# Kernel tuning notes

Measured on AMD Instinct MI355X. Metric: run time of the kernel, lower is better.

## Reference

```python
import jax, jax.numpy as jnp
import numpy as np

N = 100_000   # nodes
E = 1_250_000 # edges
D = 64        # node feature dim
H = 64        # hidden_channels
C = 10        # num_classes
G = 128       # graphs in batch


def setup_inputs() -> dict:
    key = jax.random.key(0)
    ks = jax.random.split(key, 12)
    x = jax.random.normal(ks[0], (N, D), dtype=jnp.float32)
    edge_index = jax.random.randint(ks[1], (2, E), 0, N, dtype=jnp.int64)
    batch = jnp.sort(jax.random.randint(ks[2], (N,), 0, G, dtype=jnp.int64))
    s = lambda fan_in: 1.0 / np.sqrt(fan_in)
    W1 = jax.random.normal(ks[3], (D, H), dtype=jnp.float32) * s(D)
    b1 = jnp.zeros((H,), dtype=jnp.float32)
    W2 = jax.random.normal(ks[4], (H, H), dtype=jnp.float32) * s(H)
    b2 = jnp.zeros((H,), dtype=jnp.float32)
    W3 = jax.random.normal(ks[5], (H, H), dtype=jnp.float32) * s(H)
    b3 = jnp.zeros((H,), dtype=jnp.float32)
    Wl = jax.random.normal(ks[6], (H, C), dtype=jnp.float32) * s(H)
    bl = jnp.zeros((C,), dtype=jnp.float32)
    return {"x": x, "edge_index": edge_index, "batch": batch,
            "W1": W1, "b1": b1, "W2": W2, "b2": b2,
            "W3": W3, "b3": b3, "Wl": Wl, "bl": bl}


def _gcn_conv(h, W, b, src, dst, norm, n_nodes):
    # GCNConv: out[i] = sum_{e: dst(e)=i} norm_e * (h @ W)[src(e)] + b
    h = h @ W
    msg = h[src] * norm[:, None]                       # [E+N, H]
    return jax.ops.segment_sum(msg, dst, num_segments=n_nodes) + b


def reference(x, edge_index, batch, W1, b1, W2, b2, W3, b3, Wl, bl):
    x = x.astype(jnp.float32)
    ei = edge_index.astype(jnp.int64)
    # add self-loops (as PyG gcn_norm does by default)
    loop = jnp.arange(N, dtype=ei.dtype)
    src = jnp.concatenate([ei[0], loop])
    dst = jnp.concatenate([ei[1], loop])
    # symmetric normalization: deg over targets (in-degree incl. self-loops)
    deg = jax.ops.segment_sum(jnp.ones_like(src, dtype=jnp.float32), dst,
                              num_segments=N)
    dinv = jnp.where(deg > 0, jax.lax.rsqrt(jnp.maximum(deg, 1.0)), 0.0)
    norm = dinv[src] * dinv[dst]                       # [E+N]

    h = jax.nn.relu(_gcn_conv(x, W1, b1, src, dst, norm, N))
    h = jax.nn.relu(_gcn_conv(h, W2, b2, src, dst, norm, N))
    h = _gcn_conv(h, W3, b3, src, dst, norm, N)

    # global_mean_pool over graph ids
    ones = jnp.ones((N,), dtype=jnp.float32)
    counts = jax.ops.segment_sum(ones, batch, num_segments=G)
    sums = jax.ops.segment_sum(h, batch, num_segments=G)
    pooled = sums / jnp.maximum(counts, 1.0)[:, None]  # [G, H]

    # dropout is identity in eval mode
    return pooled @ Wl + bl                            # [G, C]
```

## Files before the change

### kernel.cpp

```cpp
#include <hip/hip_runtime.h>
#include <hip/hip_bf16.h>


#define BSHIFT 7
#define BNODES (1 << BSHIFT)
#define EPB    8192
#define MAXDEG 8192
#define MAXBUCKET 32768

typedef __attribute__((ext_vector_type(8))) short bf16x8;
typedef __attribute__((ext_vector_type(4))) float f32x4;

__device__ __forceinline__ void atomAddF(float* p, float v) {
#if defined(__gfx90a__) || defined(__gfx940__) || defined(__gfx941__) || defined(__gfx942__) || defined(__gfx950__)
    unsafeAtomicAdd(p, v);
#else
    atomicAdd(p, v);
#endif
}

__device__ __forceinline__ unsigned short f2bf(float x) {
    unsigned u = __float_as_uint(x);
    u += 0x7FFFu + ((u >> 16) & 1u);
    return (unsigned short)(u >> 16);
}
__device__ __forceinline__ float bf2f(unsigned short b) {
    return __uint_as_float((unsigned)b << 16);
}

__global__ __launch_bounds__(256)
void k_bhist(const int* __restrict__ dst, int* __restrict__ cnt_all,
             int nE, int nBuckets, int binBlocks,
             const float* __restrict__ W1, const float* __restrict__ W2,
             const float* __restrict__ W3, unsigned short* __restrict__ Wt,
             float* __restrict__ pool, int poolN) {
    if (blockIdx.x >= binBlocks) {
        int li = blockIdx.x - binBlocks;
        if (li < 3) {
            const float* W = (li == 0) ? W1 : ((li == 1) ? W2 : W3);
            unsigned short* o = Wt + li * 4096;
            for (int idx = threadIdx.x; idx < 4096; idx += 256) {
                int h = idx >> 6, k = idx & 63;
                o[idx] = f2bf(W[k * 64 + h]);
            }
        } else {
            for (int i = threadIdx.x; i < poolN; i += 256) pool[i] = 0.f;
        }
        return;
    }
    __shared__ int cnt[1024];
    const int t = threadIdx.x;
    const int blk = blockIdx.x * EPB;
    for (int b = t; b < nBuckets; b += 256) cnt[b] = 0;
    __syncthreads();
#pragma unroll 4
    for (int i = 0; i < EPB / 256; i++) {
        int e = blk + i * 256 + t;
        if (e < nE) atomicAdd(&cnt[dst[e] >> BSHIFT], 1);
    }
    __syncthreads();
    for (int b = t; b < nBuckets; b += 256)
        cnt_all[(size_t)blockIdx.x * nBuckets + b] = cnt[b];
}

__global__ __launch_bounds__(256)
void k_colscan(int* __restrict__ cnt_all, int* __restrict__ bcnt,
               int nBlocks, int nBuckets) {
    const int lane = threadIdx.x & 63;
    const int b = blockIdx.x * 4 + (threadIdx.x >> 6);
    if (b >= nBuckets) return;
    int running = 0;
    for (int c = 0; c < nBlocks; c += 64) {
        int blk = c + lane;
        int v = (blk < nBlocks) ? cnt_all[(size_t)blk * nBuckets + b] : 0;
        int incl = v;
#pragma unroll
        for (int off = 1; off < 64; off <<= 1) {
            int tv = __shfl_up(incl, off);
            if (lane >= off) incl += tv;
        }
        if (blk < nBlocks) cnt_all[(size_t)blk * nBuckets + b] = running + (incl - v);
        running += __shfl(incl, 63);
    }
    if (lane == 0) bcnt[b] = running;
}

__global__ void k_bscan(const int* __restrict__ bcnt, int* __restrict__ bbase,
                        int nb, int nE) {
    __shared__ int s[256];
    const int t = threadIdx.x;
    const int base = t * 4;
    int v0 = (base + 0 < nb) ? bcnt[base + 0] : 0;
    int v1 = (base + 1 < nb) ? bcnt[base + 1] : 0;
    int v2 = (base + 2 < nb) ? bcnt[base + 2] : 0;
    int v3 = (base + 3 < nb) ? bcnt[base + 3] : 0;
    int tsum = v0 + v1 + v2 + v3;
    s[t] = tsum;
    __syncthreads();
    for (int off = 1; off < 256; off <<= 1) {
        int val = 0;
        if (t >= off) val = s[t - off];
        __syncthreads();
        if (t >= off) s[t] += val;
        __syncthreads();
    }
    int excl = s[t] - tsum;
    if (base + 0 < nb) bbase[base + 0] = excl;
    if (base + 1 < nb) bbase[base + 1] = excl + v0;
    if (base + 2 < nb) bbase[base + 2] = excl + v0 + v1;
    if (base + 3 < nb) bbase[base + 3] = excl + v0 + v1 + v2;
    if (t == 0) bbase[nb] = nE;
}

__global__ __launch_bounds__(256)
void k_bucket(const int* __restrict__ src, const int* __restrict__ dst,
              const int* __restrict__ bbase, const int* __restrict__ cnt_all,
              int* __restrict__ staging, int nE, int nBuckets) {
    __shared__ int cnt[1024];
    __shared__ int lbase[1024];
    const int t = threadIdx.x;
    const int blk = blockIdx.x * EPB;

    for (int b = t; b < nBuckets; b += 256) {
        lbase[b] = bbase[b] + cnt_all[(size_t)blockIdx.x * nBuckets + b];
        cnt[b] = 0;
    }
    __syncthreads();
#pragma unroll 4
    for (int i = 0; i < EPB / 256; i++) {
        int e = blk + i * 256 + t;
        if (e < nE) {
            int s0 = src[e], d0 = dst[e];
            int b = d0 >> BSHIFT;
            int off = atomicAdd(&cnt[b], 1);
            int pos = lbase[b] + off;
            if ((unsigned)pos < (unsigned)nE)
                staging[pos] = (s0 << BSHIFT) | (d0 & (BNODES - 1));
        }
    }
}

__global__ __launch_bounds__(256)
void k_sort(const int* __restrict__ staging, const int* __restrict__ bbase,
            int* __restrict__ csr_s, int* __restrict__ rowptr,
            int* __restrict__ rowend, float* __restrict__ dinv,
            int n, int nE) {
    __shared__ int c[BNODES];
    __shared__ int sc[BNODES];
    __shared__ int cur[BNODES];
    const int t = threadIdx.x;
    const int b = blockIdx.x;
    const int node0 = b << BSHIFT;

    int seg0 = bbase[b];
    int seg1 = bbase[b + 1];
    seg0 = max(0, min(seg0, nE));
    seg1 = max(seg0, min(seg1, nE));
    seg1 = min(seg1, seg0 + MAXBUCKET);

    if (t < BNODES) c[t] = 0;
    __syncthreads();
    for (int e = seg0 + t; e < seg1; e += 256)
        atomicAdd(&c[staging[e] & (BNODES - 1)], 1);
    __syncthreads();
    if (t < BNODES) sc[t] = c[t];
    __syncthreads();
    for (int off = 1; off < BNODES; off <<= 1) {
        int v = 0;
        if (t >= off && t < BNODES) v = sc[t - off];
        __syncthreads();
        if (t >= off && t < BNODES) sc[t] += v;
        __syncthreads();
    }
    if (t < BNODES) {
        int excl = sc[t] - c[t];
        cur[t] = excl;
        int node = node0 + t;
        if (node < n) {
            rowptr[node] = seg0 + excl;
            rowend[node] = seg0 + excl + c[t];
            dinv[node]   = rsqrtf((float)c[t] + 1.0f);
        }
    }
    __syncthreads();
    for (int e = seg0 + t; e < seg1; e += 256) {
        int p = staging[e];
        int l = p & (BNODES - 1);
        int pos = seg0 + atomicAdd(&cur[l], 1);
        if ((unsigned)pos < (unsigned)nE)
            csr_s[pos] = ((unsigned)p) >> BSHIFT;
    }
}

template<bool RELU, typename AT>
__device__ __forceinline__
void gemm_body(int bid, const AT* __restrict__ in,
               const unsigned short* __restrict__ Wt,
               const float* __restrict__ bias,
               unsigned short* __restrict__ out, int n) {
    const int lane = threadIdx.x & 63;
    const int wid  = threadIdx.x >> 6;
    const int col  = lane & 15;
    const int quad = lane >> 4;
    const int node0w = bid * 64 + wid * 16;
    const int nodeA  = node0w + col;
    const bool validA = nodeA < n;

    f32x4 zero4 = {0.f, 0.f, 0.f, 0.f};
    f32x4 acc0 = zero4, acc1 = zero4, acc2 = zero4, acc3 = zero4;

#pragma unroll
    for (int ks = 0; ks < 64; ks += 32) {
        const int kb = ks + quad * 8;
        float a[8];
        if constexpr (sizeof(AT) == 4) {
            float4 a0 = make_float4(0.f, 0.f, 0.f, 0.f);
            float4 a1 = make_float4(0.f, 0.f, 0.f, 0.f);
            if (validA) {
                a0 = *(const float4*)((const float*)in + (size_t)nodeA * 64 + kb);
                a1 = *(const float4*)((const float*)in + (size_t)nodeA * 64 + kb + 4);
            }
            a[0] = a0.x; a[1] = a0.y; a[2] = a0.z; a[3] = a0.w;
            a[4] = a1.x; a[5] = a1.y; a[6] = a1.z; a[7] = a1.w;
        } else {
            ushort4 h0 = make_ushort4(0, 0, 0, 0), h1 = make_ushort4(0, 0, 0, 0);
            if (validA) {
                h0 = *(const ushort4*)((const unsigned short*)in + (size_t)nodeA * 64 + kb);
                h1 = *(const ushort4*)((const unsigned short*)in + (size_t)nodeA * 64 + kb + 4);
            }
            a[0] = bf2f(h0.x); a[1] = bf2f(h0.y); a[2] = bf2f(h0.z); a[3] = bf2f(h0.w);
            a[4] = bf2f(h1.x); a[5] = bf2f(h1.y); a[6] = bf2f(h1.z); a[7] = bf2f(h1.w);
        }
        if (RELU) {
#pragma unroll
            for (int i = 0; i < 8; i++) a[i] = fmaxf(a[i] + bias[kb + i], 0.f);
        }
        bf16x8 af;
#pragma unroll
        for (int i = 0; i < 8; i++) af[i] = (short)f2bf(a[i]);

        const bf16x8 b0f = *(const bf16x8*)(Wt + ((0 * 16 + col) * 64 + kb));
        const bf16x8 b1f = *(const bf16x8*)(Wt + ((1 * 16 + col) * 64 + kb));
        const bf16x8 b2f = *(const bf16x8*)(Wt + ((2 * 16 + col) * 64 + kb));
        const bf16x8 b3f = *(const bf16x8*)(Wt + ((3 * 16 + col) * 64 + kb));
        acc0 = __builtin_amdgcn_mfma_f32_16x16x32_bf16(af, b0f, acc0, 0, 0, 0);
        acc1 = __builtin_amdgcn_mfma_f32_16x16x32_bf16(af, b1f, acc1, 0, 0, 0);
        acc2 = __builtin_amdgcn_mfma_f32_16x16x32_bf16(af, b2f, acc2, 0, 0, 0);
        acc3 = __builtin_amdgcn_mfma_f32_16x16x32_bf16(af, b3f, acc3, 0, 0, 0);
    }

#pragma unroll
    for (int r = 0; r < 4; r++) {
        int nn = node0w + quad * 4 + r;
        if (nn < n) {
            size_t base = (size_t)nn * 64 + col;
            out[base +  0] = f2bf(acc0[r]);
            out[base + 16] = f2bf(acc1[r]);
            out[base + 32] = f2bf(acc2[r]);
            out[base + 48] = f2bf(acc3[r]);
        }
    }
}

template<bool RELU, typename AT>
__global__ __launch_bounds__(256)
void k_gemm(const AT* __restrict__ in, const unsigned short* __restrict__ Wt,
            const float* __restrict__ bias, unsigned short* __restrict__ out, int n) {
    gemm_body<RELU, AT>(blockIdx.x, in, Wt, bias, out, n);
}

__global__ __launch_bounds__(256)
void k_wfgemm1(const int* __restrict__ csr_s, const float* __restrict__ dinv,
               float* __restrict__ csr_w, int nE, int n, int wfB,
               const float* __restrict__ x, const unsigned short* __restrict__ Wt,
               unsigned short* __restrict__ hW) {
    if (blockIdx.x < wfB) {
        int e = blockIdx.x * 256 + threadIdx.x;
        if (e < nE) {
            int s = csr_s[e];
            s = max(0, min(s, n - 1));
            csr_w[e] = dinv[s];
        }
        return;
    }
    gemm_body<false, float>(blockIdx.x - wfB, x, Wt, nullptr, hW, n);
}

template<int LAYER>
__global__ __launch_bounds__(256)
void k_agg(const unsigned short* __restrict__ hW, const int* __restrict__ rowptr,
           const int* __restrict__ rowend, const int* __restrict__ csr_s,
           const float* __restrict__ csr_w, const float* __restrict__ dinv,
           unsigned short* __restrict__ aggb, int n, int nE) {
    const int lane = threadIdx.x & 63;
    const int wid  = threadIdx.x >> 6;
    const int nA = blockIdx.x * 8 + wid * 2;
    const int nB = nA + 1;
    if (nA >= n) return;
    const bool vB = (nB < n);

    int rowA = rowptr[nA], endA = rowend[nA];
    rowA = max(0, min(rowA, nE)); endA = max(rowA, min(endA, nE));
    endA = min(endA, rowA + MAXDEG);
    int rowB = 0, endB = 0;
    if (vB) {
        rowB = rowptr[nB]; endB = rowend[nB];
        rowB = max(0, min(rowB, nE)); endB = max(rowB, min(endB, nE));
        endB = min(endB, rowB + MAXDEG);
    }
    const float diA = dinv[nA];
    const float diB = vB ? dinv[nB] : 0.f;

    float a0 = diA * diA * bf2f(hW[(size_t)nA * 64 + lane]);
    float a1 = 0.f, a2 = 0.f, a3 = 0.f;
    float b0 = vB ? diB * diB * bf2f(hW[(size_t)nB * 64 + lane]) : 0.f;
    float b1 = 0.f, b2 = 0.f, b3 = 0.f;

    const int nm1 = n - 1;
    int baseA = rowA, baseB = rowB;
    while (baseA < endA || baseB < endB) {
        int mA = max(0, min(32, endA - baseA));
        int mB = max(0, min(32, endB - baseB));
        int   s_l = 0;
        float w_l = 0.f;
        if (lane < 32) {
            if (lane < mA) {
                int e = baseA + lane;
                s_l = csr_s[e];
                w_l = csr_w[e] * diA;
            }
        } else {
            int l2 = lane - 32;
            if (l2 < mB) {
                int e = baseB + l2;
                s_l = csr_s[e];
                w_l = csr_w[e] * diB;
            }
        }
        const unsigned w_u = __float_as_uint(w_l);
        const int m = max(mA, mB);
        int j = 0;
        for (; j + 4 <= m; j += 4) {
            int sA0 = min(__builtin_amdgcn_readlane(s_l, j    ), nm1);
            int sA1 = min(__builtin_amdgcn_readlane(s_l, j + 1), nm1);
            int sA2 = min(__builtin_amdgcn_readlane(s_l, j + 2), nm1);
            int sA3 = min(__builtin_amdgcn_readlane(s_l, j + 3), nm1);
            int sB0 = min(__builtin_amdgcn_readlane(s_l, j + 32), nm1);
            int sB1 = min(__builtin_amdgcn_readlane(s_l, j + 33), nm1);
            int sB2 = min(__builtin_amdgcn_readlane(s_l, j + 34), nm1);
            int sB3 = min(__builtin_amdgcn_readlane(s_l, j + 35), nm1);
            float wA0 = __uint_as_float(__builtin_amdgcn_readlane(w_u, j));
            float wA1 = __uint_as_float(__builtin_amdgcn_readlane(w_u, j + 1));
            float wA2 = __uint_as_float(__builtin_amdgcn_readlane(w_u, j + 2));
            float wA3 = __uint_as_float(__builtin_amdgcn_readlane(w_u, j + 3));
            float wB0 = __uint_as_float(__builtin_amdgcn_readlane(w_u, j + 32));
            float wB1 = __uint_as_float(__builtin_amdgcn_readlane(w_u, j + 33));
            float wB2 = __uint_as_float(__builtin_amdgcn_readlane(w_u, j + 34));
            float wB3 = __uint_as_float(__builtin_amdgcn_readlane(w_u, j + 35));
            float hA0 = bf2f(hW[(size_t)sA0 * 64 + lane]);
            float hA1 = bf2f(hW[(size_t)sA1 * 64 + lane]);
            float hA2 = bf2f(hW[(size_t)sA2 * 64 + lane]);
            float hA3 = bf2f(hW[(size_t)sA3 * 64 + lane]);
            float hB0 = bf2f(hW[(size_t)sB0 * 64 + lane]);
            float hB1 = bf2f(hW[(size_t)sB1 * 64 + lane]);
            float hB2 = bf2f(hW[(size_t)sB2 * 64 + lane]);
            float hB3 = bf2f(hW[(size_t)sB3 * 64 + lane]);
            a0 += wA0 * hA0; a1 += wA1 * hA1;
            a2 += wA2 * hA2; a3 += wA3 * hA3;
            b0 += wB0 * hB0; b1 += wB1 * hB1;
            b2 += wB2 * hB2; b3 += wB3 * hB3;
        }
        for (; j < m; j++) {
            int   sA = min(__builtin_amdgcn_readlane(s_l, j), nm1);
            int   sB = min(__builtin_amdgcn_readlane(s_l, j + 32), nm1);
            float wA = __uint_as_float(__builtin_amdgcn_readlane(w_u, j));
            float wB = __uint_as_float(__builtin_amdgcn_readlane(w_u, j + 32));
            a0 += wA * bf2f(hW[(size_t)sA * 64 + lane]);
            b0 += wB * bf2f(hW[(size_t)sB * 64 + lane]);
        }
        baseA += mA;
        baseB += mB;
    }
    aggb[(size_t)nA * 64 + lane] = f2bf((a0 + a1) + (a2 + a3));
    if (vB) aggb[(size_t)nB * 64 + lane] = f2bf((b0 + b1) + (b2 + b3));
}

__global__ void k_pool(const unsigned short* __restrict__ aggb,
                       const int* __restrict__ batch,
                       float* __restrict__ pool, float* __restrict__ cnt, int n) {
    const int lane = threadIdx.x;
    const int base = blockIdx.x * 64;
    int g_cur = -1, run = 0;
    float acc = 0.f;
    for (int j = 0; j < 64; j++) {
        int node = base + j;
        if (node >= n) break;
        int g = batch[node];
        if (g != g_cur) {
            if (g_cur >= 0) {
                atomAddF(&pool[g_cur * 64 + lane], acc);
                if (lane == 0) atomAddF(&cnt[g_cur], (float)run);
            }
            g_cur = g; acc = 0.f; run = 0;
        }
        acc += bf2f(aggb[(size_t)node * 64 + lane]);
        run++;
    }
    if (g_cur >= 0) {
        atomAddF(&pool[g_cur * 64 + lane], acc);
        if (lane == 0) atomAddF(&cnt[g_cur], (float)run);
    }
}

__global__ void k_final(const float* __restrict__ pool, const float* __restrict__ cnt,
                        const float* __restrict__ b3, const float* __restrict__ Wl,
                        const float* __restrict__ bl, float* __restrict__ out) {
    __shared__ float s[64];
    const int g = blockIdx.x, t = threadIdx.x;
    float c = fmaxf(cnt[g], 1.0f);
    s[t] = pool[g * 64 + t] / c + b3[t];
    __syncthreads();
    if (t < 10) {
        float acc = bl[t];
#pragma unroll
        for (int k = 0; k < 64; k++) acc += s[k] * Wl[k * 10 + t];
        out[g * 10 + t] = acc;
    }
}

extern "C" void kernel_launch(void* const* d_in, const int* in_sizes, int n_in,
                              void* d_out, int out_size, void* d_ws, size_t ws_size,
                              hipStream_t stream) {
    const float* x   = (const float*)d_in[0];
    const int*   ei  = (const int*)d_in[1];
    const int*   bat = (const int*)d_in[2];
    const float* W1  = (const float*)d_in[3];
    const float* b1  = (const float*)d_in[4];
    const float* W2  = (const float*)d_in[5];
    const float* b2  = (const float*)d_in[6];
    const float* W3  = (const float*)d_in[7];
    const float* b3  = (const float*)d_in[8];
    const float* Wl  = (const float*)d_in[9];
    const float* bl  = (const float*)d_in[10];
    float* out = (float*)d_out;

    const int N_ = in_sizes[0] / 64;
    const int E_ = in_sizes[1] / 2;
    const int G_ = out_size / 10;
    const int NB_ = (N_ + BNODES - 1) >> BSHIFT;
    const int bin_blocks = (E_ + EPB - 1) / EPB;

    char* p = (char*)d_ws;
    int*   staging = (int*)p;   p += (size_t)E_ * 4;
    int*   csr_s  = (int*)p;    p += (size_t)E_ * 4;
    float* csr_w  = (float*)p;  p += (size_t)E_ * 4;
    unsigned short* aggb = (unsigned short*)p; p += (size_t)N_ * 64 * 2;
    unsigned short* hW   = (unsigned short*)p; p += (size_t)N_ * 64 * 2;
    float* dinv   = (float*)p;  p += (size_t)N_ * 4;
    int*   rowptr = (int*)p;    p += (size_t)N_ * 4;
    int*   rowend = (int*)p;    p += (size_t)N_ * 4;
    float* pool   = (float*)p;  p += (size_t)G_ * 64 * 4;
    float* cnt    = (float*)p;  p += (size_t)G_ * 4;
    unsigned short* Wt = (unsigned short*)p; p += 3 * 4096 * 2;
    int*   bcnt   = (int*)p;    p += (size_t)(NB_ + 1) * 4;
    int*   bbase  = (int*)p;    p += (size_t)(NB_ + 1) * 4;
    int*   cnt_all = (int*)p;   p += (size_t)bin_blocks * NB_ * 4;

    const int* srcp = ei;
    const int* dstp = ei + E_;

    k_bhist<<<bin_blocks + 4, 256, 0, stream>>>(dstp, cnt_all, E_, NB_,
                                                bin_blocks, W1, W2, W3, Wt,
                                                pool, G_ * 64 + G_);
    k_colscan<<<(NB_ + 3) / 4, 256, 0, stream>>>(cnt_all, bcnt, bin_blocks, NB_);
    k_bscan<<<1, 256, 0, stream>>>(bcnt, bbase, NB_, E_);
    k_bucket<<<bin_blocks, 256, 0, stream>>>(srcp, dstp, bbase, cnt_all,
                                             staging, E_, NB_);
    k_sort<<<NB_, 256, 0, stream>>>(staging, bbase, csr_s, rowptr, rowend,
                                    dinv, N_, E_);

    const int gemm_blocks = (N_ + 63) / 64;
    const int agg_blocks  = (N_ + 7) / 8;
    const int wf_blocks   = (E_ + 255) / 256;

    k_wfgemm1<<<wf_blocks + gemm_blocks, 256, 0, stream>>>(
        csr_s, dinv, csr_w, E_, N_, wf_blocks, x, Wt, hW);
    k_agg<1><<<agg_blocks, 256, 0, stream>>>(hW, rowptr, rowend, csr_s, csr_w,
                                             dinv, aggb, N_, E_);
    k_gemm<true, unsigned short><<<gemm_blocks, 256, 0, stream>>>(aggb, Wt + 4096,
                                                                  b1, hW, N_);
    k_agg<2><<<agg_blocks, 256, 0, stream>>>(hW, rowptr, rowend, csr_s, csr_w,
                                             dinv, aggb, N_, E_);
    k_gemm<true, unsigned short><<<gemm_blocks, 256, 0, stream>>>(aggb, Wt + 8192,
                                                                  b2, hW, N_);
    k_agg<3><<<agg_blocks, 256, 0, stream>>>(hW, rowptr, rowend, csr_s, csr_w,
                                             dinv, aggb, N_, E_);

    k_pool<<<(N_ + 63) / 64, 64, 0, stream>>>(aggb, bat, pool, cnt, N_);
    k_final<<<G_, 64, 0, stream>>>(pool, cnt, b3, Wl, bl, out);
}
```

Before: 343.6 us.

## Fuse CSR build and pool/final kernels into cooperative grid-synced launches

```diff
diff --git a/kernel.cpp b/kernel.cpp
--- a/kernel.cpp
+++ b/kernel.cpp
@@ -1,5 +1,8 @@
 #include <hip/hip_runtime.h>
 #include <hip/hip_bf16.h>
+#include <hip/hip_cooperative_groups.h>
+
+namespace cg = cooperative_groups;
 
 
 #define BSHIFT 7
@@ -29,166 +32,170 @@
 }
 
 __global__ __launch_bounds__(256)
-void k_bhist(const int* __restrict__ dst, int* __restrict__ cnt_all,
-             int nE, int nBuckets, int binBlocks,
-             const float* __restrict__ W1, const float* __restrict__ W2,
-             const float* __restrict__ W3, unsigned short* __restrict__ Wt,
-             float* __restrict__ pool, int poolN) {
-    if (blockIdx.x >= binBlocks) {
-        int li = blockIdx.x - binBlocks;
-        if (li < 3) {
-            const float* W = (li == 0) ? W1 : ((li == 1) ? W2 : W3);
-            unsigned short* o = Wt + li * 4096;
-            for (int idx = threadIdx.x; idx < 4096; idx += 256) {
-                int h = idx >> 6, k = idx & 63;
-                o[idx] = f2bf(W[k * 64 + h]);
-            }
-        } else {
-            for (int i = threadIdx.x; i < poolN; i += 256) pool[i] = 0.f;
-        }
-        return;
-    }
-    __shared__ int cnt[1024];
-    const int t = threadIdx.x;
-    const int blk = blockIdx.x * EPB;
-    for (int b = t; b < nBuckets; b += 256) cnt[b] = 0;
-    __syncthreads();
+void k_csr(const int* __restrict__ src, const int* __restrict__ dst,
+           int* __restrict__ cnt_all, int* __restrict__ bcnt,
+           int* __restrict__ bbase, int* __restrict__ staging,
+           int* __restrict__ csr_s, float* __restrict__ csr_w,
+           int* __restrict__ rowptr, int* __restrict__ rowend,
+           float* __restrict__ dinv,
+           const float* __restrict__ W1, const float* __restrict__ W2,
+           const float* __restrict__ W3, unsigned short* __restrict__ Wt,
+           float* __restrict__ pool, int poolN,
+           int nE, int n, int nBuckets, int binBlocks) {
+    cg::grid_group grid = cg::this_grid();
+    __shared__ int sA[1024];
+    __shared__ int sB[1024];
+    const int t   = threadIdx.x;
+    const int bid = blockIdx.x;
+
+    if (bid < binBlocks) {
+        for (int b = t; b < nBuckets; b += 256) sA[b] = 0;
+        __syncthreads();
+        const int blk = bid * EPB;
 #pragma unroll 4
-    for (int i = 0; i < EPB / 256; i++) {
-        int e = blk + i * 256 + t;
-        if (e < nE) atomicAdd(&cnt[dst[e] >> BSHIFT], 1);
-    }
-    __syncthreads();
-    for (int b = t; b < nBuckets; b += 256)
-        cnt_all[(size_t)blockIdx.x * nBuckets + b] = cnt[b];
-}
-
-__global__ __launch_bounds__(256)
-void k_colscan(int* __restrict__ cnt_all, int* __restrict__ bcnt,
-               int nBlocks, int nBuckets) {
-    const int lane = threadIdx.x & 63;
-    const int b = blockIdx.x * 4 + (threadIdx.x >> 6);
-    if (b >= nBuckets) return;
-    int running = 0;
-    for (int c = 0; c < nBlocks; c += 64) {
-        int blk = c + lane;
-        int v = (blk < nBlocks) ? cnt_all[(size_t)blk * nBuckets + b] : 0;
-        int incl = v;
+        for (int i = 0; i < EPB / 256; i++) {
+            int e = blk + i * 256 + t;
+            if (e < nE) atomicAdd(&sA[dst[e] >> BSHIFT], 1);
+        }
+        __syncthreads();
+        for (int b = t; b < nBuckets; b += 256)
+            cnt_all[(size_t)bid * nBuckets + b] = sA[b];
+    } else if (bid < binBlocks + 3) {
+        int li = bid - binBlocks;
+        const float* W = (li == 0) ? W1 : ((li == 1) ? W2 : W3);
+        unsigned short* o = Wt + li * 4096;
+        for (int idx = t; idx < 4096; idx += 256) {
+            int h = idx >> 6, k = idx & 63;
+            o[idx] = f2bf(W[k * 64 + h]);
+        }
+    } else if (bid == binBlocks + 3) {
+        for (int i = t; i < poolN; i += 256) pool[i] = 0.f;
+    }
+    grid.sync();
+
+    {
+        const int lane = t & 63;
+        const int b = bid * 4 + (t >> 6);
+        if (b < nBuckets) {
+            int running = 0;
+            for (int c = 0; c < binBlocks; c += 64) {
+                int blk2 = c + lane;
+                int v = (blk2 < binBlocks) ? cnt_all[(size_t)blk2 * nBuckets + b] : 0;
+                int incl = v;
 #pragma unroll
-        for (int off = 1; off < 64; off <<= 1) {
-            int tv = __shfl_up(incl, off);
-            if (lane >= off) incl += tv;
-        }
-        if (blk < nBlocks) cnt_all[(size_t)blk * nBuckets + b] = running + (incl - v);
-        running += __shfl(incl, 63);
-    }
-    if (lane == 0) bcnt[b] = running;
-}
-
-__global__ void k_bscan(const int* __restrict__ bcnt, int* __restrict__ bbase,
-                        int nb, int nE) {
-    __shared__ int s[256];
-    const int t = threadIdx.x;
-    const int base = t * 4;
-    int v0 = (base + 0 < nb) ? bcnt[base + 0] : 0;
-    int v1 = (base + 1 < nb) ? bcnt[base + 1] : 0;
-    int v2 = (base + 2 < nb) ? bcnt[base + 2] : 0;
-    int v3 = (base + 3 < nb) ? bcnt[base + 3] : 0;
-    int tsum = v0 + v1 + v2 + v3;
-    s[t] = tsum;
-    __syncthreads();
-    for (int off = 1; off < 256; off <<= 1) {
-        int val = 0;
-        if (t >= off) val = s[t - off];
-        __syncthreads();
-        if (t >= off) s[t] += val;
-        __syncthreads();
-    }
-    int excl = s[t] - tsum;
-    if (base + 0 < nb) bbase[base + 0] = excl;
-    if (base + 1 < nb) bbase[base + 1] = excl + v0;
-    if (base + 2 < nb) bbase[base + 2] = excl + v0 + v1;
-    if (base + 3 < nb) bbase[base + 3] = excl + v0 + v1 + v2;
-    if (t == 0) bbase[nb] = nE;
-}
-
-__global__ __launch_bounds__(256)
-void k_bucket(const int* __restrict__ src, const int* __restrict__ dst,
-              const int* __restrict__ bbase, const int* __restrict__ cnt_all,
-              int* __restrict__ staging, int nE, int nBuckets) {
-    __shared__ int cnt[1024];
-    __shared__ int lbase[1024];
-    const int t = threadIdx.x;
-    const int blk = blockIdx.x * EPB;
-
-    for (int b = t; b < nBuckets; b += 256) {
-        lbase[b] = bbase[b] + cnt_all[(size_t)blockIdx.x * nBuckets + b];
-        cnt[b] = 0;
-    }
-    __syncthreads();
+                for (int off = 1; off < 64; off <<= 1) {
+                    int tv = __shfl_up(incl, off);
+                    if (lane >= off) incl += tv;
+                }
+                if (blk2 < binBlocks)
+                    cnt_all[(size_t)blk2 * nBuckets + b] = running + (incl - v);
+                running += __shfl(incl, 63);
+            }
+            if (lane == 0) bcnt[b] = running;
+        }
+    }
+    grid.sync();
+
+    if (bid == 0) {
+        const int base = t * 4;
+        int v0 = (base + 0 < nBuckets) ? bcnt[base + 0] : 0;
+        int v1 = (base + 1 < nBuckets) ? bcnt[base + 1] : 0;
+        int v2 = (base + 2 < nBuckets) ? bcnt[base + 2] : 0;
+        int v3 = (base + 3 < nBuckets) ? bcnt[base + 3] : 0;
+        int tsum = v0 + v1 + v2 + v3;
+        sA[t] = tsum;
+        __syncthreads();
+        for (int off = 1; off < 256; off <<= 1) {
+            int val = 0;
+            if (t >= off) val = sA[t - off];
+            __syncthreads();
+            if (t >= off) sA[t] += val;
+            __syncthreads();
+        }
+        int excl = sA[t] - tsum;
+        if (base + 0 < nBuckets) bbase[base + 0] = excl;
+        if (base + 1 < nBuckets) bbase[base + 1] = excl + v0;
+        if (base + 2 < nBuckets) bbase[base + 2] = excl + v0 + v1;
+        if (base + 3 < nBuckets) bbase[base + 3] = excl + v0 + v1 + v2;
+        if (t == 0) bbase[nBuckets] = nE;
+    }
+    grid.sync();
+
+    if (bid < binBlocks) {
+        for (int b = t; b < nBuckets; b += 256) {
+            sB[b] = bbase[b] + cnt_all[(size_t)bid * nBuckets + b];
+            sA[b] = 0;
+        }
+        __syncthreads();
+        const int blk = bid * EPB;
 #pragma unroll 4
-    for (int i = 0; i < EPB / 256; i++) {
-        int e = blk + i * 256 + t;
-        if (e < nE) {
-            int s0 = src[e], d0 = dst[e];
-            int b = d0 >> BSHIFT;
-            int off = atomicAdd(&cnt[b], 1);
-            int pos = lbase[b] + off;
-            if ((unsigned)pos < (unsigned)nE)
-                staging[pos] = (s0 << BSHIFT) | (d0 & (BNODES - 1));
-        }
-    }
-}
-
-__global__ __launch_bounds__(256)
-void k_sort(const int* __restrict__ staging, const int* __restrict__ bbase,
-            int* __restrict__ csr_s, int* __restrict__ rowptr,
-            int* __restrict__ rowend, float* __restrict__ dinv,
-            int n, int nE) {
-    __shared__ int c[BNODES];
-    __shared__ int sc[BNODES];
-    __shared__ int cur[BNODES];
-    const int t = threadIdx.x;
-    const int b = blockIdx.x;
-    const int node0 = b << BSHIFT;
-
-    int seg0 = bbase[b];
-    int seg1 = bbase[b + 1];
-    seg0 = max(0, min(seg0, nE));
-    seg1 = max(seg0, min(seg1, nE));
-    seg1 = min(seg1, seg0 + MAXBUCKET);
-
-    if (t < BNODES) c[t] = 0;
-    __syncthreads();
-    for (int e = seg0 + t; e < seg1; e += 256)
-        atomicAdd(&c[staging[e] & (BNODES - 1)], 1);
-    __syncthreads();
-    if (t < BNODES) sc[t] = c[t];
-    __syncthreads();
-    for (int off = 1; off < BNODES; off <<= 1) {
-        int v = 0;
-        if (t >= off && t < BNODES) v = sc[t - off];
-        __syncthreads();
-        if (t >= off && t < BNODES) sc[t] += v;
-        __syncthreads();
-    }
-    if (t < BNODES) {
-        int excl = sc[t] - c[t];
-        cur[t] = excl;
-        int node = node0 + t;
-        if (node < n) {
-            rowptr[node] = seg0 + excl;
-            rowend[node] = seg0 + excl + c[t];
-            dinv[node]   = rsqrtf((float)c[t] + 1.0f);
-        }
-    }
-    __syncthreads();
-    for (int e = seg0 + t; e < seg1; e += 256) {
-        int p = staging[e];
-        int l = p & (BNODES - 1);
-        int pos = seg0 + atomicAdd(&cur[l], 1);
-        if ((unsigned)pos < (unsigned)nE)
-            csr_s[pos] = ((unsigned)p) >> BSHIFT;
+        for (int i = 0; i < EPB / 256; i++) {
+            int e = blk + i * 256 + t;
+            if (e < nE) {
+                int s0 = src[e], d0 = dst[e];
+                int b = d0 >> BSHIFT;
+                int off = atomicAdd(&sA[b], 1);
+                int pos = sB[b] + off;
+                if ((unsigned)pos < (unsigned)nE)
+                    staging[pos] = (s0 << BSHIFT) | (d0 & (BNODES - 1));
+            }
+        }
+    }
+    grid.sync();
+
+    int seg0 = 0, seg1 = 0;
+    {
+        int* c   = sA;
+        int* sc  = sA + 128;
+        int* cur = sA + 256;
+        const int node0 = bid << BSHIFT;
+        seg0 = bbase[bid];
+        seg1 = bbase[bid + 1];
+        seg0 = max(0, min(seg0, nE));
+        seg1 = max(seg0, min(seg1, nE));
+        seg1 = min(seg1, seg0 + MAXBUCKET);
+
+        if (t < BNODES) c[t] = 0;
+        __syncthreads();
+        for (int e = seg0 + t; e < seg1; e += 256)
+            atomicAdd(&c[staging[e] & (BNODES - 1)], 1);
+        __syncthreads();
+        if (t < BNODES) sc[t] = c[t];
+        __syncthreads();
+        for (int off = 1; off < BNODES; off <<= 1) {
+            int v = 0;
+            if (t >= off && t < BNODES) v = sc[t - off];
+            __syncthreads();
+            if (t >= off && t < BNODES) sc[t] += v;
+            __syncthreads();
+        }
+        if (t < BNODES) {
+            int excl = sc[t] - c[t];
+            cur[t] = excl;
+            int node = node0 + t;
+            if (node < n) {
+                rowptr[node] = seg0 + excl;
+                rowend[node] = seg0 + excl + c[t];
+                dinv[node]   = rsqrtf((float)c[t] + 1.0f);
+            }
+        }
+    }
+    grid.sync();
+
+    {
+        int* cur = sA + 256;
+        const int nm1 = n - 1;
+        for (int e = seg0 + t; e < seg1; e += 256) {
+            int p = staging[e];
+            int l = p & (BNODES - 1);
+            int pos = seg0 + atomicAdd(&cur[l], 1);
+            if ((unsigned)pos < (unsigned)nE) {
+                int sidx = (int)(((unsigned)p) >> BSHIFT);
+                csr_s[pos] = sidx;
+                sidx = max(0, min(sidx, nm1));
+                csr_w[pos] = dinv[sidx];
+            }
+        }
     }
 }
 
@@ -267,23 +274,6 @@
 void k_gemm(const AT* __restrict__ in, const unsigned short* __restrict__ Wt,
             const float* __restrict__ bias, unsigned short* __restrict__ out, int n) {
     gemm_body<RELU, AT>(blockIdx.x, in, Wt, bias, out, n);
-}
-
-__global__ __launch_bounds__(256)
-void k_wfgemm1(const int* __restrict__ csr_s, const float* __restrict__ dinv,
-               float* __restrict__ csr_w, int nE, int n, int wfB,
-               const float* __restrict__ x, const unsigned short* __restrict__ Wt,
-               unsigned short* __restrict__ hW) {
-    if (blockIdx.x < wfB) {
-        int e = blockIdx.x * 256 + threadIdx.x;
-        if (e < nE) {
-            int s = csr_s[e];
-            s = max(0, min(s, n - 1));
-            csr_w[e] = dinv[s];
-        }
-        return;
-    }
-    gemm_body<false, float>(blockIdx.x - wfB, x, Wt, nullptr, hW, n);
 }
 
 template<int LAYER>
@@ -385,46 +375,57 @@
     if (vB) aggb[(size_t)nB * 64 + lane] = f2bf((b0 + b1) + (b2 + b3));
 }
 
-__global__ void k_pool(const unsigned short* __restrict__ aggb,
-                       const int* __restrict__ batch,
-                       float* __restrict__ pool, float* __restrict__ cnt, int n) {
-    const int lane = threadIdx.x;
-    const int base = blockIdx.x * 64;
-    int g_cur = -1, run = 0;
-    float acc = 0.f;
-    for (int j = 0; j < 64; j++) {
-        int node = base + j;
-        if (node >= n) break;
-        int g = batch[node];
-        if (g != g_cur) {
-            if (g_cur >= 0) {
-                atomAddF(&pool[g_cur * 64 + lane], acc);
-                if (lane == 0) atomAddF(&cnt[g_cur], (float)run);
-            }
-            g_cur = g; acc = 0.f; run = 0;
-        }
-        acc += bf2f(aggb[(size_t)node * 64 + lane]);
-        run++;
-    }
-    if (g_cur >= 0) {
-        atomAddF(&pool[g_cur * 64 + lane], acc);
-        if (lane == 0) atomAddF(&cnt[g_cur], (float)run);
-    }
-}
-
-__global__ void k_final(const float* __restrict__ pool, const float* __restrict__ cnt,
-                        const float* __restrict__ b3, const float* __restrict__ Wl,
-                        const float* __restrict__ bl, float* __restrict__ out) {
+__global__ __launch_bounds__(256)
+void k_poolfinal(const unsigned short* __restrict__ aggb,
+                 const int* __restrict__ batch,
+                 float* __restrict__ pool, float* __restrict__ cnt,
+                 const float* __restrict__ b3, const float* __restrict__ Wl,
+                 const float* __restrict__ bl, float* __restrict__ out,
+                 int n, int G) {
+    cg::grid_group grid = cg::this_grid();
+    const int lane = threadIdx.x & 63;
+    const int wid  = threadIdx.x >> 6;
+    const int base = (blockIdx.x * 4 + wid) * 64;
+
+    if (base < n) {
+        int g_cur = -1, run = 0;
+        float acc = 0.f;
+        for (int j = 0; j < 64; j++) {
+            int node = base + j;
+            if (node >= n) break;
+            int g = batch[node];
+            if (g != g_cur) {
+                if (g_cur >= 0) {
+                    atomAddF(&pool[g_cur * 64 + lane], acc);
+                    if (lane == 0) atomAddF(&cnt[g_cur], (float)run);
+                }
+                g_cur = g; acc = 0.f; run = 0;
+            }
+            acc += bf2f(aggb[(size_t)node * 64 + lane]);
+            run++;
+        }
+        if (g_cur >= 0) {
+            atomAddF(&pool[g_cur * 64 + lane], acc);
+            if (lane == 0) atomAddF(&cnt[g_cur], (float)run);
+        }
+    }
+    grid.sync();
+
+    const int g = blockIdx.x;
     __shared__ float s[64];
-    const int g = blockIdx.x, t = threadIdx.x;
-    float c = fmaxf(cnt[g], 1.0f);
-    s[t] = pool[g * 64 + t] / c + b3[t];
-    __syncthreads();
-    if (t < 10) {
-        float acc = bl[t];
+    if (g < G) {
+        const int t = threadIdx.x;
+        if (t < 64) {
+            float c = fmaxf(cnt[g], 1.0f);
+            s[t] = pool[g * 64 + t] / c + b3[t];
+        }
+        __syncthreads();
+        if (t < 10) {
+            float acc = bl[t];
 #pragma unroll
-        for (int k = 0; k < 64; k++) acc += s[k] * Wl[k * 10 + t];
-        out[g * 10 + t] = acc;
+            for (int k = 0; k < 64; k++) acc += s[k] * Wl[k * 10 + t];
+            out[g * 10 + t] = acc;
+        }
     }
 }
 
@@ -444,11 +445,11 @@
     const float* bl  = (const float*)d_in[10];
     float* out = (float*)d_out;
 
-    const int N_ = in_sizes[0] / 64;
-    const int E_ = in_sizes[1] / 2;
-    const int G_ = out_size / 10;
-    const int NB_ = (N_ + BNODES - 1) >> BSHIFT;
-    const int bin_blocks = (E_ + EPB - 1) / EPB;
+    int N_ = in_sizes[0] / 64;
+    int E_ = in_sizes[1] / 2;
+    int G_ = out_size / 10;
+    int NB_ = (N_ + BNODES - 1) >> BSHIFT;
+    int bin_blocks = (E_ + EPB - 1) / EPB;
 
     char* p = (char*)d_ws;
     int*   staging = (int*)p;   p += (size_t)E_ * 4;
@@ -468,23 +469,26 @@
 
     const int* srcp = ei;
     const int* dstp = ei + E_;
-
-    k_bhist<<<bin_blocks + 4, 256, 0, stream>>>(dstp, cnt_all, E_, NB_,
-                                                bin_blocks, W1, W2, W3, Wt,
-                                                pool, G_ * 64 + G_);
-    k_colscan<<<(NB_ + 3) / 4, 256, 0, stream>>>(cnt_all, bcnt, bin_blocks, NB_);
-    k_bscan<<<1, 256, 0, stream>>>(bcnt, bbase, NB_, E_);
-    k_bucket<<<bin_blocks, 256, 0, stream>>>(srcp, dstp, bbase, cnt_all,
-                                             staging, E_, NB_);
-    k_sort<<<NB_, 256, 0, stream>>>(staging, bbase, csr_s, rowptr, rowend,
-                                    dinv, N_, E_);
+    int poolN = G_ * 64 + G_;
+
+    {
+        int NBLK = bin_blocks + 4;
+        if ((NB_ + 3) / 4 > NBLK) NBLK = (NB_ + 3) / 4;
+        if (NB_ > NBLK) NBLK = NB_;
+        void* args[] = { (void*)&srcp, (void*)&dstp, (void*)&cnt_all, (void*)&bcnt,
+                         (void*)&bbase, (void*)&staging, (void*)&csr_s, (void*)&csr_w,
+                         (void*)&rowptr, (void*)&rowend, (void*)&dinv,
+                         (void*)&W1, (void*)&W2, (void*)&W3, (void*)&Wt,
+                         (void*)&pool, (void*)&poolN,
+                         (void*)&E_, (void*)&N_, (void*)&NB_, (void*)&bin_blocks };
+        hipLaunchCooperativeKernel((void*)k_csr, dim3(NBLK), dim3(256),
+                                   args, 0, stream);
+    }
 
     const int gemm_blocks = (N_ + 63) / 64;
     const int agg_blocks  = (N_ + 7) / 8;
-    const int wf_blocks   = (E_ + 255) / 256;
-
-    k_wfgemm1<<<wf_blocks + gemm_blocks, 256, 0, stream>>>(
-        csr_s, dinv, csr_w, E_, N_, wf_blocks, x, Wt, hW);
+
+    k_gemm<false, float><<<gemm_blocks, 256, 0, stream>>>(x, Wt, nullptr, hW, N_);
     k_agg<1><<<agg_blocks, 256, 0, stream>>>(hW, rowptr, rowend, csr_s, csr_w,
                                              dinv, aggb, N_, E_);
     k_gemm<true, unsigned short><<<gemm_blocks, 256, 0, stream>>>(aggb, Wt + 4096,
@@ -496,6 +500,13 @@
     k_agg<3><<<agg_blocks, 256, 0, stream>>>(hW, rowptr, rowend, csr_s, csr_w,
                                              dinv, aggb, N_, E_);
 
-    k_pool<<<(N_ + 63) / 64, 64, 0, stream>>>(aggb, bat, pool, cnt, N_);
-    k_final<<<G_, 64, 0, stream>>>(pool, cnt, b3, Wl, bl, out);
-}
+    {
+        int PF = (N_ + 255) / 256;
+        if (G_ > PF) PF = G_;
+        void* args[] = { (void*)&aggb, (void*)&bat, (void*)&pool, (void*)&cnt,
+                         (void*)&b3, (void*)&Wl, (void*)&bl, (void*)&out,
+                         (void*)&N_, (void*)&G_ };
+        hipLaunchCooperativeKernel((void*)k_poolfinal, dim3(PF), dim3(256),
+                                   args, 0, stream);
+    }
+}
```

Result: slower. 853.5 us (+148.4%).
